# Kernel optimization log

Hardware: AMD Instinct MI355X
Metric: run time of the kernel (lower is better)

Reference implementation:

```python
import jax, jax.numpy as jnp
import numpy as np
from jax import lax

PIXEL_MAX = 255.0  # PSNR reference intensity, matches I=255 in the torch source


def setup_inputs() -> dict:
    key = jax.random.key(0)
    k1, k2 = jax.random.split(key)
    # RGBA image and RGBA kernel, 0..255 pixel range (PSNR uses I=255)
    x = jax.random.uniform(k1, (1, 4, 2048, 2048), dtype=jnp.float32) * PIXEL_MAX
    kernel = jax.random.uniform(k2, (1, 4, 16, 16), dtype=jnp.float32) * PIXEL_MAX
    return {"x": x, "kernel": kernel}


def reference(x, kernel):
    """Fused equivalent of: unfold every (Hk,Wk) window, alpha-blend it with the
    kernel using the kernel's alpha channel, then per-window PSNR vs the kernel.

    alpha_blend(x_win, k, a) = (1-a)*x_win + a*k  with a = k_alpha/255, so
    blended - k = (1-a)*(x_win - k), hence per-window per-channel MSE is a
    weighted sliding-window sum: mean_ij w_ij*(x-k)^2 with w = (1-a)^2.
    Expanding (x-k)^2 lets us use three depthwise VALID correlations instead of
    materializing the [L,C,Hk,Wk] unfold+repeat tensor.
    """
    C, Hk, Wk = kernel.shape[1], kernel.shape[2], kernel.shape[3]
    k = kernel[0]                       # (C, Hk, Wk)
    alpha = k[3] / PIXEL_MAX            # (Hk, Wk), alpha plane (channel 3)
    w = (1.0 - alpha) ** 2              # per-tap weight, shared across channels

    dn = ("NCHW", "OIHW", "NCHW")
    w_dw = jnp.broadcast_to(w, (C, 1, Hk, Wk))   # depthwise weights
    kw_dw = (k * w)[:, None]                      # (C, 1, Hk, Wk)

    def corr(inp, wt):
        return lax.conv_general_dilated(
            inp, wt, window_strides=(1, 1), padding="VALID",
            dimension_numbers=dn, feature_group_count=C)

    Sxx = corr(x * x, w_dw)                        # (1, C, H', W') sum w*x^2
    Sxk = corr(x, kw_dw)                           # (1, C, H', W') sum w*x*k
    Skk = jnp.sum(k * k * w, axis=(-2, -1))[None, :, None, None]  # sum w*k^2

    mse = (Sxx - 2.0 * Sxk + Skk) / (Hk * Wk)      # (1, C, H', W')
    psnr = jnp.mean(20.0 * jnp.log10(PIXEL_MAX / jnp.sqrt(mse)), axis=1)  # mean over C
    return psnr[0]                                  # (H-Hk+1, W-Wk+1)
```

## Files before the change

kernel.cpp:

```cpp
#include <hip/hip_runtime.h>
#include <hip/hip_bf16.h>
#include <math.h>

#define XDIM 2048
#define OW   2033
#define TR   32
#define TC   256
#define NIP  47
#define XW   272

typedef __bf16 bf16x8 __attribute__((ext_vector_type(8)));
typedef float  f32x16 __attribute__((ext_vector_type(16)));

union U128 { uint4 u; bf16x8 v; };

__device__ __forceinline__ unsigned short bfbits(float f) {
    return __builtin_bit_cast(unsigned short, __float2bfloat16(f));
}
__device__ __forceinline__ unsigned int packx(float f) {
    return ((unsigned int)bfbits(f) << 16) | (unsigned int)bfbits(f * f);
}

__global__ __launch_bounds__(256) void psnr_mfma_kernel(
    const float* __restrict__ x,
    const float* __restrict__ kern,
    float* __restrict__ out)
{
    __shared__ __align__(16) unsigned int xt[NIP * XW];
    __shared__ __align__(16) unsigned int wt[4][17][20];
    __shared__ float skkArr[4];

    const int tid  = threadIdx.x;
    const int lane = tid & 63;
    const int wv   = tid >> 6;
    const int nn   = lane & 31;
    const int hf   = lane >> 5;

    {
        float k0 = kern[tid], k1 = kern[256 + tid], k2 = kern[512 + tid], k3 = kern[768 + tid];
        float a  = k3 * (1.0f / 255.0f);
        float om = 1.0f - a;
        float w  = om * om;
        int i = tid >> 4, j = tid & 15;
        unsigned int wlo = (unsigned int)bfbits(w);
        wt[0][i][j] = ((unsigned int)bfbits(-2.0f * w * k0) << 16) | wlo;
        wt[1][i][j] = ((unsigned int)bfbits(-2.0f * w * k1) << 16) | wlo;
        wt[2][i][j] = ((unsigned int)bfbits(-2.0f * w * k2) << 16) | wlo;
        wt[3][i][j] = ((unsigned int)bfbits(-2.0f * w * k3) << 16) | wlo;
        if (tid < 80) {
            int c = tid / 20, wd = tid % 20;
            wt[c][16][wd] = 0u;
        }
        float4* red = reinterpret_cast<float4*>(xt);
        red[tid] = make_float4(w*k0*k0, w*k1*k1, w*k2*k2, w*k3*k3);
        __syncthreads();
        #pragma unroll
        for (int s = 128; s > 0; s >>= 1) {
            if (tid < s) {
                float4 o = red[tid + s], m = red[tid];
                m.x += o.x; m.y += o.y; m.z += o.z; m.w += o.w;
                red[tid] = m;
            }
            __syncthreads();
        }
        if (tid == 0) {
            float4 r0v = red[0];
            skkArr[0] = r0v.x; skkArr[1] = r0v.y; skkArr[2] = r0v.z; skkArr[3] = r0v.w;
        }
    }

    const int r0 = blockIdx.y * TR;
    const int c0 = blockIdx.x * TC;

    f32x16 psum0 = {0.f}, psum1 = {0.f};
    #pragma unroll
    for (int q = 0; q < 16; ++q) { psum0[q] = 0.0f; psum1[q] = 0.0f; }

    for (int ch = 0; ch < 4; ++ch) {
        __syncthreads();
        const float* __restrict__ xc = x + (size_t)ch * XDIM * XDIM;
        for (int idx = tid; idx < NIP * 68; idx += 256) {
            int row = idx / 68;
            int q4  = (idx - row * 68) * 4;
            int gr  = r0 + row; if (gr > XDIM - 1) gr = XDIM - 1;
            int gc  = c0 + q4;
            const float* rp = xc + (size_t)gr * XDIM;
            float4 v;
            if (gc + 3 <= XDIM - 1) {
                v = *reinterpret_cast<const float4*>(rp + gc);
            } else {
                int e0 = gc     < XDIM ? gc     : XDIM - 1;
                int e1 = gc + 1 < XDIM ? gc + 1 : XDIM - 1;
                int e2 = gc + 2 < XDIM ? gc + 2 : XDIM - 1;
                int e3 = gc + 3 < XDIM ? gc + 3 : XDIM - 1;
                v = make_float4(rp[e0], rp[e1], rp[e2], rp[e3]);
            }
            uint4 pr;
            pr.x = packx(v.x); pr.y = packx(v.y); pr.z = packx(v.z); pr.w = packx(v.w);
            *reinterpret_cast<uint4*>(&xt[row * XW + q4]) = pr;
        }
        __syncthreads();

        f32x16 acc0 = {0.f}, acc1 = {0.f};
        #pragma unroll
        for (int q = 0; q < 16; ++q) { acc0[q] = 0.0f; acc1[q] = 0.0f; }

        for (int ip = 0; ip < NIP; ++ip) {
            unsigned int d = (unsigned int)(ip - nn);
            unsigned int wrow = (d > 15u) ? 16u : d;
            U128 alo, ahi;
            alo.u = *reinterpret_cast<const uint4*>(&wt[ch][wrow][hf * 4]);
            ahi.u = *reinterpret_cast<const uint4*>(&wt[ch][wrow][8 + hf * 4]);

            int xb = ip * XW + nn + hf * 4 + (wv << 6);
            U128 blo0, bhi0, blo1, bhi1;
            blo0.u = make_uint4(xt[xb],      xt[xb + 1],  xt[xb + 2],  xt[xb + 3]);
            bhi0.u = make_uint4(xt[xb + 8],  xt[xb + 9],  xt[xb + 10], xt[xb + 11]);
            blo1.u = make_uint4(xt[xb + 32], xt[xb + 33], xt[xb + 34], xt[xb + 35]);
            bhi1.u = make_uint4(xt[xb + 40], xt[xb + 41], xt[xb + 42], xt[xb + 43]);

            acc0 = __builtin_amdgcn_mfma_f32_32x32x16_bf16(alo.v, blo0.v, acc0, 0, 0, 0);
            acc0 = __builtin_amdgcn_mfma_f32_32x32x16_bf16(ahi.v, bhi0.v, acc0, 0, 0, 0);
            acc1 = __builtin_amdgcn_mfma_f32_32x32x16_bf16(alo.v, blo1.v, acc1, 0, 0, 0);
            acc1 = __builtin_amdgcn_mfma_f32_32x32x16_bf16(ahi.v, bhi1.v, acc1, 0, 0, 0);
        }

        float sk = skkArr[ch];
        #pragma unroll
        for (int q = 0; q < 16; ++q) {
            float m0 = (acc0[q] + sk) * (1.0f / 256.0f);
            float m1 = (acc1[q] + sk) * (1.0f / 256.0f);
            psum0[q] += log10f(m0);
            psum1[q] += log10f(m1);
        }
    }

    const float BASE = 48.130803608679344f;
    const int col0 = c0 + (wv << 6) + nn;
    const int col1 = col0 + 32;
    #pragma unroll
    for (int q = 0; q < 16; ++q) {
        int row = r0 + (q & 3) + ((q >> 2) << 3) + (hf << 2);
        if (row < OW) {
            float* orow = out + (size_t)row * OW;
            if (col0 < OW) orow[col0] = BASE - 2.5f * psum0[q];
            if (col1 < OW) orow[col1] = BASE - 2.5f * psum1[q];
        }
    }
}

extern "C" void kernel_launch(void* const* d_in, const int* in_sizes, int n_in,
                              void* d_out, int out_size, void* d_ws, size_t ws_size,
                              hipStream_t stream) {
    (void)in_sizes; (void)n_in; (void)d_ws; (void)ws_size; (void)out_size;
    const float* x    = (const float*)d_in[0];
    const float* kern = (const float*)d_in[1];
    float* out        = (float*)d_out;

    dim3 grid(XDIM / TC, (OW + TR - 1) / TR);
    psnr_mfma_kernel<<<grid, 256, 0, stream>>>(x, kern, out);
}
```

Measured before the change: 70.61 us.

## Pipeline input staging through triple-buffered row chunks with register prefetch

Replaces the per-channel load-everything-then-compute scheme with 8-row chunks staged through a triple-buffered LDS ring. Global loads for chunk g+3 are issued into registers while chunk g+2 is packed into LDS and chunk g runs MFMA, so memory latency overlaps compute. The LDS layout also changes to pre-duplicated uint2 pairs, so each B operand is built from two 64-bit reads instead of four scalar reads. In exchange it adds a barrier per chunk, more register pressure from the prefetch buffers, and somewhat more LDS write traffic because values are duplicated.

```diff
diff --git a/kernel.cpp b/kernel.cpp
--- a/kernel.cpp
+++ b/kernel.cpp
@@ -6,8 +6,10 @@
 #define OW   2033
 #define TR   32
 #define TC   256
-#define NIP  47
 #define XW   272
+#define CH   8
+#define NCHUNK 6
+#define NG   24
 
 typedef __bf16 bf16x8 __attribute__((ext_vector_type(8)));
 typedef float  f32x16 __attribute__((ext_vector_type(16)));
@@ -26,7 +28,7 @@
     const float* __restrict__ kern,
     float* __restrict__ out)
 {
-    __shared__ __align__(16) unsigned int xt[NIP * XW];
+    __shared__ __align__(16) uint2 bufT[3][CH][XW];
     __shared__ __align__(16) unsigned int wt[4][17][20];
     __shared__ float skkArr[4];
 
@@ -51,7 +53,7 @@
             int c = tid / 20, wd = tid % 20;
             wt[c][16][wd] = 0u;
         }
-        float4* red = reinterpret_cast<float4*>(xt);
+        float4* red = reinterpret_cast<float4*>(&bufT[0][0][0]);
         red[tid] = make_float4(w*k0*k0, w*k1*k1, w*k2*k2, w*k3*k3);
         __syncthreads();
         #pragma unroll
@@ -67,72 +69,127 @@
             float4 r0v = red[0];
             skkArr[0] = r0v.x; skkArr[1] = r0v.y; skkArr[2] = r0v.z; skkArr[3] = r0v.w;
         }
+        __syncthreads();
     }
 
     const int r0 = blockIdx.y * TR;
     const int c0 = blockIdx.x * TC;
 
-    f32x16 psum0 = {0.f}, psum1 = {0.f};
+    float4 sv4[2][3];
+    float  sv1[2][3];
+
+    auto stage_issue = [&](int g, int rs) {
+        int c  = g % NCHUNK;
+        int ch = g / NCHUNK;
+        const float* __restrict__ xc = x + (size_t)ch * XDIM * XDIM;
+        #pragma unroll
+        for (int t = 0; t < 3; ++t) {
+            int idx = tid + 256 * t;
+            if (idx < CH * 68) {
+                int lr = idx / 68;
+                int q4 = (idx - lr * 68) * 4;
+                int gr = r0 + c * CH + lr; if (gr > XDIM - 1) gr = XDIM - 1;
+                int gc = c0 + q4;
+                const float* rp = xc + (size_t)gr * XDIM;
+                float4 v;
+                if (gc + 3 <= XDIM - 1) {
+                    v = *reinterpret_cast<const float4*>(rp + gc);
+                } else {
+                    int e0 = gc     < XDIM ? gc     : XDIM - 1;
+                    int e1 = gc + 1 < XDIM ? gc + 1 : XDIM - 1;
+                    int e2 = gc + 2 < XDIM ? gc + 2 : XDIM - 1;
+                    int e3 = gc + 3 < XDIM ? gc + 3 : XDIM - 1;
+                    v = make_float4(rp[e0], rp[e1], rp[e2], rp[e3]);
+                }
+                int g4 = gc + 4 < XDIM ? gc + 4 : XDIM - 1;
+                sv4[rs][t] = v;
+                sv1[rs][t] = rp[g4];
+            }
+        }
+    };
+
+    auto stage_write = [&](int g, int rs) {
+        int b = g % 3;
+        #pragma unroll
+        for (int t = 0; t < 3; ++t) {
+            int idx = tid + 256 * t;
+            if (idx < CH * 68) {
+                int lr = idx / 68;
+                int q4 = (idx - lr * 68) * 4;
+                float4 v = sv4[rs][t];
+                unsigned int P0 = packx(v.x), P1 = packx(v.y), P2 = packx(v.z),
+                             P3 = packx(v.w), P4 = packx(sv1[rs][t]);
+                uint4* dst = reinterpret_cast<uint4*>(&bufT[b][lr][q4]);
+                dst[0] = make_uint4(P0, P1, P1, P2);
+                dst[1] = make_uint4(P2, P3, P3, P4);
+            }
+        }
+    };
+
+    stage_issue(0, 0);
+    stage_issue(1, 1);
+    stage_write(0, 0);
+    stage_issue(2, 0);
+    stage_write(1, 1);
+    __syncthreads();
+
+    f32x16 acc0, acc1, psum0, psum1;
     #pragma unroll
     for (int q = 0; q < 16; ++q) { psum0[q] = 0.0f; psum1[q] = 0.0f; }
 
-    for (int ch = 0; ch < 4; ++ch) {
+    const int xbase = nn + 4 * hf + (wv << 6);
+
+    for (int g = 0; g < NG; ++g) {
+        const int c  = g % NCHUNK;
+        const int ch = g / NCHUNK;
+
+        if (g + 2 < NG) stage_write(g + 2, g & 1);
+        if (g + 3 < NG) stage_issue(g + 3, (g + 1) & 1);
+
+        if (c == 0) {
+            #pragma unroll
+            for (int q = 0; q < 16; ++q) { acc0[q] = 0.0f; acc1[q] = 0.0f; }
+        }
+
+        const uint2* __restrict__ bp = &bufT[g % 3][0][0];
+        const unsigned int* __restrict__ wch = &wt[ch][0][0];
+
+        #pragma unroll
+        for (int lr = 0; lr < CH; ++lr) {
+            int ip = c * CH + lr;
+            if (ip < 47) {
+                unsigned int d = (unsigned int)(ip - nn);
+                unsigned int wrow = (d > 15u) ? 16u : d;
+                U128 alo, ahi;
+                alo.u = *reinterpret_cast<const uint4*>(wch + wrow * 20 + hf * 4);
+                ahi.u = *reinterpret_cast<const uint4*>(wch + wrow * 20 + 8 + hf * 4);
+
+                int xb = lr * XW + xbase;
+                U128 blo0, bhi0, blo1, bhi1;
+                { uint2 a0 = bp[xb],      a1 = bp[xb + 2];  blo0.u = make_uint4(a0.x, a0.y, a1.x, a1.y); }
+                { uint2 a0 = bp[xb + 8],  a1 = bp[xb + 10]; bhi0.u = make_uint4(a0.x, a0.y, a1.x, a1.y); }
+                { uint2 a0 = bp[xb + 32], a1 = bp[xb + 34]; blo1.u = make_uint4(a0.x, a0.y, a1.x, a1.y); }
+                { uint2 a0 = bp[xb + 40], a1 = bp[xb + 42]; bhi1.u = make_uint4(a0.x, a0.y, a1.x, a1.y); }
+
+                acc0 = __builtin_amdgcn_mfma_f32_32x32x16_bf16(alo.v, blo0.v, acc0, 0, 0, 0);
+                acc0 = __builtin_amdgcn_mfma_f32_32x32x16_bf16(ahi.v, bhi0.v, acc0, 0, 0, 0);
+                acc1 = __builtin_amdgcn_mfma_f32_32x32x16_bf16(alo.v, blo1.v, acc1, 0, 0, 0);
+                acc1 = __builtin_amdgcn_mfma_f32_32x32x16_bf16(ahi.v, bhi1.v, acc1, 0, 0, 0);
+            }
+        }
+
+        if (c == NCHUNK - 1) {
+            float sk = skkArr[ch];
+            #pragma unroll
+            for (int q = 0; q < 16; ++q) {
+                float m0 = (acc0[q] + sk) * (1.0f / 256.0f);
+                float m1 = (acc1[q] + sk) * (1.0f / 256.0f);
+                psum0[q] += log10f(m0);
+                psum1[q] += log10f(m1);
+            }
+        }
+
         __syncthreads();
-        const float* __restrict__ xc = x + (size_t)ch * XDIM * XDIM;
-        for (int idx = tid; idx < NIP * 68; idx += 256) {
-            int row = idx / 68;
-            int q4  = (idx - row * 68) * 4;
-            int gr  = r0 + row; if (gr > XDIM - 1) gr = XDIM - 1;
-            int gc  = c0 + q4;
-            const float* rp = xc + (size_t)gr * XDIM;
-            float4 v;
-            if (gc + 3 <= XDIM - 1) {
-                v = *reinterpret_cast<const float4*>(rp + gc);
-            } else {
-                int e0 = gc     < XDIM ? gc     : XDIM - 1;
-                int e1 = gc + 1 < XDIM ? gc + 1 : XDIM - 1;
-                int e2 = gc + 2 < XDIM ? gc + 2 : XDIM - 1;
-                int e3 = gc + 3 < XDIM ? gc + 3 : XDIM - 1;
-                v = make_float4(rp[e0], rp[e1], rp[e2], rp[e3]);
-            }
-            uint4 pr;
-            pr.x = packx(v.x); pr.y = packx(v.y); pr.z = packx(v.z); pr.w = packx(v.w);
-            *reinterpret_cast<uint4*>(&xt[row * XW + q4]) = pr;
-        }
-        __syncthreads();
-
-        f32x16 acc0 = {0.f}, acc1 = {0.f};
-        #pragma unroll
-        for (int q = 0; q < 16; ++q) { acc0[q] = 0.0f; acc1[q] = 0.0f; }
-
-        for (int ip = 0; ip < NIP; ++ip) {
-            unsigned int d = (unsigned int)(ip - nn);
-            unsigned int wrow = (d > 15u) ? 16u : d;
-            U128 alo, ahi;
-            alo.u = *reinterpret_cast<const uint4*>(&wt[ch][wrow][hf * 4]);
-            ahi.u = *reinterpret_cast<const uint4*>(&wt[ch][wrow][8 + hf * 4]);
-
-            int xb = ip * XW + nn + hf * 4 + (wv << 6);
-            U128 blo0, bhi0, blo1, bhi1;
-            blo0.u = make_uint4(xt[xb],      xt[xb + 1],  xt[xb + 2],  xt[xb + 3]);
-            bhi0.u = make_uint4(xt[xb + 8],  xt[xb + 9],  xt[xb + 10], xt[xb + 11]);
-            blo1.u = make_uint4(xt[xb + 32], xt[xb + 33], xt[xb + 34], xt[xb + 35]);
-            bhi1.u = make_uint4(xt[xb + 40], xt[xb + 41], xt[xb + 42], xt[xb + 43]);
-
-            acc0 = __builtin_amdgcn_mfma_f32_32x32x16_bf16(alo.v, blo0.v, acc0, 0, 0, 0);
-            acc0 = __builtin_amdgcn_mfma_f32_32x32x16_bf16(ahi.v, bhi0.v, acc0, 0, 0, 0);
-            acc1 = __builtin_amdgcn_mfma_f32_32x32x16_bf16(alo.v, blo1.v, acc1, 0, 0, 0);
-            acc1 = __builtin_amdgcn_mfma_f32_32x32x16_bf16(ahi.v, bhi1.v, acc1, 0, 0, 0);
-        }
-
-        float sk = skkArr[ch];
-        #pragma unroll
-        for (int q = 0; q < 16; ++q) {
-            float m0 = (acc0[q] + sk) * (1.0f / 256.0f);
-            float m1 = (acc1[q] + sk) * (1.0f / 256.0f);
-            psum0[q] += log10f(m0);
-            psum1[q] += log10f(m1);
-        }
     }
 
     const float BASE = 48.130803608679344f;
```

New measurement: 115.3 us. 63.3% more time.

## Replace block-wide tile staging with per-wave register-prefetched LDS ring pipeline

Applied to the files above, without the earlier changes.

Drops the per-channel block-wide load of the full 47-row tile and its barriers. Each wave now streams its own 80-column slice row by row into a private 8-slot LDS ring, keeping four global loads in flight in registers while the MFMAs run on earlier rows. Channels and rows are flattened into 188 steps, and the LDS layout changes to pre-expanded uint2 pairs. The goal is to overlap global latency with MFMA work and remove block syncs. In exchange, only 20 lanes per wave issue loads and wave-local LDS reuse depends on implicit wave ordering with no explicit barrier.

```diff
diff --git a/kernel.cpp b/kernel.cpp
--- a/kernel.cpp
+++ b/kernel.cpp
@@ -6,8 +6,9 @@
 #define OW   2033
 #define TR   32
 #define TC   256
-#define NIP  47
-#define XW   272
+#define WPC  80
+#define NROW 47
+#define NG   188
 
 typedef __bf16 bf16x8 __attribute__((ext_vector_type(8)));
 typedef float  f32x16 __attribute__((ext_vector_type(16)));
@@ -26,7 +27,7 @@
     const float* __restrict__ kern,
     float* __restrict__ out)
 {
-    __shared__ __align__(16) unsigned int xt[NIP * XW];
+    __shared__ __align__(16) uint2 ring[4][8][WPC];
     __shared__ __align__(16) unsigned int wt[4][17][20];
     __shared__ float skkArr[4];
 
@@ -35,6 +36,49 @@
     const int wv   = tid >> 6;
     const int nn   = lane & 31;
     const int hf   = lane >> 5;
+
+    const int r0  = blockIdx.y * TR;
+    const int c0  = blockIdx.x * TC;
+    const int c0w = c0 + (wv << 6);
+
+    float4 s04, s14, s24, s34;
+    float  s01, s11, s21, s31;
+
+    auto issue = [&](int g, float4& v4, float& v1) {
+        int ch = (g * 1395) >> 16;
+        int ip = g - 47 * ch;
+        if (lane < 20) {
+            int gr = r0 + ip; if (gr > XDIM - 1) gr = XDIM - 1;
+            int gc = c0w + 4 * lane;
+            const float* rp = x + ((size_t)ch << 22) + (size_t)gr * XDIM;
+            if (gc + 3 <= XDIM - 1) {
+                v4 = *reinterpret_cast<const float4*>(rp + gc);
+            } else {
+                int e0 = gc     < XDIM ? gc     : XDIM - 1;
+                int e1 = gc + 1 < XDIM ? gc + 1 : XDIM - 1;
+                int e2 = gc + 2 < XDIM ? gc + 2 : XDIM - 1;
+                int e3 = gc + 3 < XDIM ? gc + 3 : XDIM - 1;
+                v4 = make_float4(rp[e0], rp[e1], rp[e2], rp[e3]);
+            }
+            int e4 = gc + 4 < XDIM ? gc + 4 : XDIM - 1;
+            v1 = rp[e4];
+        }
+    };
+
+    auto wr = [&](int g, const float4& v4, const float& v1) {
+        if (lane < 20) {
+            unsigned int P0 = packx(v4.x), P1 = packx(v4.y), P2 = packx(v4.z),
+                         P3 = packx(v4.w), P4 = packx(v1);
+            uint4* dst = reinterpret_cast<uint4*>(&ring[wv][g & 7][lane * 4]);
+            dst[0] = make_uint4(P0, P1, P1, P2);
+            dst[1] = make_uint4(P2, P3, P3, P4);
+        }
+    };
+
+    issue(0, s04, s01);
+    issue(1, s14, s11);
+    issue(2, s24, s21);
+    issue(3, s34, s31);
 
     {
         float k0 = kern[tid], k1 = kern[256 + tid], k2 = kern[512 + tid], k3 = kern[768 + tid];
@@ -51,7 +95,7 @@
             int c = tid / 20, wd = tid % 20;
             wt[c][16][wd] = 0u;
         }
-        float4* red = reinterpret_cast<float4*>(xt);
+        float4* red = reinterpret_cast<float4*>(&ring[0][0][0]);
         red[tid] = make_float4(w*k0*k0, w*k1*k1, w*k2*k2, w*k3*k3);
         __syncthreads();
         #pragma unroll
@@ -67,76 +111,76 @@
             float4 r0v = red[0];
             skkArr[0] = r0v.x; skkArr[1] = r0v.y; skkArr[2] = r0v.z; skkArr[3] = r0v.w;
         }
+        __syncthreads();
     }
 
-    const int r0 = blockIdx.y * TR;
-    const int c0 = blockIdx.x * TC;
-
-    f32x16 psum0 = {0.f}, psum1 = {0.f};
+    f32x16 acc0, acc1, psum0, psum1;
     #pragma unroll
     for (int q = 0; q < 16; ++q) { psum0[q] = 0.0f; psum1[q] = 0.0f; }
 
-    for (int ch = 0; ch < 4; ++ch) {
-        __syncthreads();
-        const float* __restrict__ xc = x + (size_t)ch * XDIM * XDIM;
-        for (int idx = tid; idx < NIP * 68; idx += 256) {
-            int row = idx / 68;
-            int q4  = (idx - row * 68) * 4;
-            int gr  = r0 + row; if (gr > XDIM - 1) gr = XDIM - 1;
-            int gc  = c0 + q4;
-            const float* rp = xc + (size_t)gr * XDIM;
-            float4 v;
-            if (gc + 3 <= XDIM - 1) {
-                v = *reinterpret_cast<const float4*>(rp + gc);
-            } else {
-                int e0 = gc     < XDIM ? gc     : XDIM - 1;
-                int e1 = gc + 1 < XDIM ? gc + 1 : XDIM - 1;
-                int e2 = gc + 2 < XDIM ? gc + 2 : XDIM - 1;
-                int e3 = gc + 3 < XDIM ? gc + 3 : XDIM - 1;
-                v = make_float4(rp[e0], rp[e1], rp[e2], rp[e3]);
+    const int xb = nn + 4 * hf;
+
+    auto compute = [&](int g) {
+        int ch = (g * 1395) >> 16;
+        int ip = g - 47 * ch;
+        if (ip == 0) {
+            #pragma unroll
+            for (int q = 0; q < 16; ++q) { acc0[q] = 0.0f; acc1[q] = 0.0f; }
+        }
+        const unsigned int* __restrict__ wch = &wt[ch][0][0];
+        unsigned int d = (unsigned int)(ip - nn);
+        unsigned int wrow = (d > 15u) ? 16u : d;
+        U128 alo, ahi;
+        alo.u = *reinterpret_cast<const uint4*>(wch + wrow * 20 + hf * 4);
+        ahi.u = *reinterpret_cast<const uint4*>(wch + wrow * 20 + 8 + hf * 4);
+
+        const uint2* __restrict__ bp = &ring[wv][g & 7][0];
+        U128 blo0, bhi0, blo1, bhi1;
+        { uint2 a0 = bp[xb],      a1 = bp[xb + 2];  blo0.u = make_uint4(a0.x, a0.y, a1.x, a1.y); }
+        { uint2 a0 = bp[xb + 8],  a1 = bp[xb + 10]; bhi0.u = make_uint4(a0.x, a0.y, a1.x, a1.y); }
+        { uint2 a0 = bp[xb + 32], a1 = bp[xb + 34]; blo1.u = make_uint4(a0.x, a0.y, a1.x, a1.y); }
+        { uint2 a0 = bp[xb + 40], a1 = bp[xb + 42]; bhi1.u = make_uint4(a0.x, a0.y, a1.x, a1.y); }
+
+        acc0 = __builtin_amdgcn_mfma_f32_32x32x16_bf16(alo.v, blo0.v, acc0, 0, 0, 0);
+        acc0 = __builtin_amdgcn_mfma_f32_32x32x16_bf16(ahi.v, bhi0.v, acc0, 0, 0, 0);
+        acc1 = __builtin_amdgcn_mfma_f32_32x32x16_bf16(alo.v, blo1.v, acc1, 0, 0, 0);
+        acc1 = __builtin_amdgcn_mfma_f32_32x32x16_bf16(ahi.v, bhi1.v, acc1, 0, 0, 0);
+
+        if (ip == NROW - 1) {
+            float sk = skkArr[ch];
+            #pragma unroll
+            for (int q = 0; q < 16; ++q) {
+                float m0 = (acc0[q] + sk) * (1.0f / 256.0f);
+                float m1 = (acc1[q] + sk) * (1.0f / 256.0f);
+                psum0[q] += log10f(m0);
+                psum1[q] += log10f(m1);
             }
-            uint4 pr;
-            pr.x = packx(v.x); pr.y = packx(v.y); pr.z = packx(v.z); pr.w = packx(v.w);
-            *reinterpret_cast<uint4*>(&xt[row * XW + q4]) = pr;
-        }
-        __syncthreads();
-
-        f32x16 acc0 = {0.f}, acc1 = {0.f};
-        #pragma unroll
-        for (int q = 0; q < 16; ++q) { acc0[q] = 0.0f; acc1[q] = 0.0f; }
-
-        for (int ip = 0; ip < NIP; ++ip) {
-            unsigned int d = (unsigned int)(ip - nn);
-            unsigned int wrow = (d > 15u) ? 16u : d;
-            U128 alo, ahi;
-            alo.u = *reinterpret_cast<const uint4*>(&wt[ch][wrow][hf * 4]);
-            ahi.u = *reinterpret_cast<const uint4*>(&wt[ch][wrow][8 + hf * 4]);
-
-            int xb = ip * XW + nn + hf * 4 + (wv << 6);
-            U128 blo0, bhi0, blo1, bhi1;
-            blo0.u = make_uint4(xt[xb],      xt[xb + 1],  xt[xb + 2],  xt[xb + 3]);
-            bhi0.u = make_uint4(xt[xb + 8],  xt[xb + 9],  xt[xb + 10], xt[xb + 11]);
-            blo1.u = make_uint4(xt[xb + 32], xt[xb + 33], xt[xb + 34], xt[xb + 35]);
-            bhi1.u = make_uint4(xt[xb + 40], xt[xb + 41], xt[xb + 42], xt[xb + 43]);
-
-            acc0 = __builtin_amdgcn_mfma_f32_32x32x16_bf16(alo.v, blo0.v, acc0, 0, 0, 0);
-            acc0 = __builtin_amdgcn_mfma_f32_32x32x16_bf16(ahi.v, bhi0.v, acc0, 0, 0, 0);
-            acc1 = __builtin_amdgcn_mfma_f32_32x32x16_bf16(alo.v, blo1.v, acc1, 0, 0, 0);
-            acc1 = __builtin_amdgcn_mfma_f32_32x32x16_bf16(ahi.v, bhi1.v, acc1, 0, 0, 0);
-        }
-
-        float sk = skkArr[ch];
-        #pragma unroll
-        for (int q = 0; q < 16; ++q) {
-            float m0 = (acc0[q] + sk) * (1.0f / 256.0f);
-            float m1 = (acc1[q] + sk) * (1.0f / 256.0f);
-            psum0[q] += log10f(m0);
-            psum1[q] += log10f(m1);
-        }
+        }
+    };
+
+    wr(0, s04, s01);
+    issue(4, s04, s01);
+
+    for (int g = 0; g < NG; g += 4) {
+        wr(g + 1, s14, s11);
+        if (g + 5 < NG) issue(g + 5, s14, s11);
+        compute(g);
+
+        wr(g + 2, s24, s21);
+        if (g + 6 < NG) issue(g + 6, s24, s21);
+        compute(g + 1);
+
+        wr(g + 3, s34, s31);
+        if (g + 7 < NG) issue(g + 7, s34, s31);
+        compute(g + 2);
+
+        if (g + 4 < NG) { wr(g + 4, s04, s01); }
+        if (g + 8 < NG) issue(g + 8, s04, s01);
+        compute(g + 3);
     }
 
     const float BASE = 48.130803608679344f;
-    const int col0 = c0 + (wv << 6) + nn;
+    const int col0 = c0w + nn;
     const int col1 = col0 + 32;
     #pragma unroll
     for (int q = 0; q < 16; ++q) {
```

After: 159.7 us. +126.2%, slower.

## Prefetch next channel's tile into registers during MFMA, use fast log2

Applied to the files above, without the earlier changes.

Global loads for the next channel's input tile now go into a 13-entry float4 register buffer and are issued before the MFMA loop of the current channel. The bf16 pack and LDS store happen at the top of the next iteration, so global memory latency overlaps with matrix compute. The per-channel log10f calls are replaced by __log2f, with the output scale folded into a constant. The register buffer adds roughly 52 VGPRs, which may lower occupancy, and __log2f is slightly less accurate.

```diff
diff --git a/kernel.cpp b/kernel.cpp
--- a/kernel.cpp
+++ b/kernel.cpp
@@ -6,8 +6,9 @@
 #define OW   2033
 #define TR   32
 #define TC   256
-#define NIP  47
 #define XW   272
+#define NIT  13
+#define NITEMS (47*68)
 
 typedef __bf16 bf16x8 __attribute__((ext_vector_type(8)));
 typedef float  f32x16 __attribute__((ext_vector_type(16)));
@@ -26,7 +27,7 @@
     const float* __restrict__ kern,
     float* __restrict__ out)
 {
-    __shared__ __align__(16) unsigned int xt[NIP * XW];
+    __shared__ __align__(16) unsigned int xt[47 * XW];
     __shared__ __align__(16) unsigned int wt[4][17][20];
     __shared__ float skkArr[4];
 
@@ -35,6 +36,51 @@
     const int wv   = tid >> 6;
     const int nn   = lane & 31;
     const int hf   = lane >> 5;
+
+    const int r0 = blockIdx.y * TR;
+    const int c0 = blockIdx.x * TC;
+
+    float4 pf[NIT];
+
+    auto issue = [&](int ch) {
+        const float* __restrict__ xc = x + ((size_t)ch << 22);
+        #pragma unroll
+        for (int t = 0; t < NIT; ++t) {
+            int idx = tid + 256 * t;
+            if (idx < NITEMS) {
+                int row = idx / 68;
+                int q4  = (idx - row * 68) * 4;
+                int gr  = r0 + row; if (gr > XDIM - 1) gr = XDIM - 1;
+                int gc  = c0 + q4;
+                const float* rp = xc + (size_t)gr * XDIM;
+                if (gc + 3 <= XDIM - 1) {
+                    pf[t] = *reinterpret_cast<const float4*>(rp + gc);
+                } else {
+                    int e0 = gc     < XDIM ? gc     : XDIM - 1;
+                    int e1 = gc + 1 < XDIM ? gc + 1 : XDIM - 1;
+                    int e2 = gc + 2 < XDIM ? gc + 2 : XDIM - 1;
+                    int e3 = gc + 3 < XDIM ? gc + 3 : XDIM - 1;
+                    pf[t] = make_float4(rp[e0], rp[e1], rp[e2], rp[e3]);
+                }
+            }
+        }
+    };
+
+    auto wrt = [&]() {
+        #pragma unroll
+        for (int t = 0; t < NIT; ++t) {
+            int idx = tid + 256 * t;
+            if (idx < NITEMS) {
+                int row = idx / 68;
+                int q4  = (idx - row * 68) * 4;
+                float4 v = pf[t];
+                *reinterpret_cast<uint4*>(&xt[row * XW + q4]) =
+                    make_uint4(packx(v.x), packx(v.y), packx(v.z), packx(v.w));
+            }
+        }
+    };
+
+    issue(0);
 
     {
         float k0 = kern[tid], k1 = kern[256 + tid], k2 = kern[512 + tid], k3 = kern[768 + tid];
@@ -51,7 +97,7 @@
             int c = tid / 20, wd = tid % 20;
             wt[c][16][wd] = 0u;
         }
-        float4* red = reinterpret_cast<float4*>(xt);
+        float4* red = reinterpret_cast<float4*>(&xt[0]);
         red[tid] = make_float4(w*k0*k0, w*k1*k1, w*k2*k2, w*k3*k3);
         __syncthreads();
         #pragma unroll
@@ -67,52 +113,34 @@
             float4 r0v = red[0];
             skkArr[0] = r0v.x; skkArr[1] = r0v.y; skkArr[2] = r0v.z; skkArr[3] = r0v.w;
         }
+        __syncthreads();
     }
 
-    const int r0 = blockIdx.y * TR;
-    const int c0 = blockIdx.x * TC;
-
-    f32x16 psum0 = {0.f}, psum1 = {0.f};
+    f32x16 psum0, psum1;
     #pragma unroll
     for (int q = 0; q < 16; ++q) { psum0[q] = 0.0f; psum1[q] = 0.0f; }
 
+    const int xbase = nn + 4 * hf + (wv << 6);
+
     for (int ch = 0; ch < 4; ++ch) {
+        wrt();
         __syncthreads();
-        const float* __restrict__ xc = x + (size_t)ch * XDIM * XDIM;
-        for (int idx = tid; idx < NIP * 68; idx += 256) {
-            int row = idx / 68;
-            int q4  = (idx - row * 68) * 4;
-            int gr  = r0 + row; if (gr > XDIM - 1) gr = XDIM - 1;
-            int gc  = c0 + q4;
-            const float* rp = xc + (size_t)gr * XDIM;
-            float4 v;
-            if (gc + 3 <= XDIM - 1) {
-                v = *reinterpret_cast<const float4*>(rp + gc);
-            } else {
-                int e0 = gc     < XDIM ? gc     : XDIM - 1;
-                int e1 = gc + 1 < XDIM ? gc + 1 : XDIM - 1;
-                int e2 = gc + 2 < XDIM ? gc + 2 : XDIM - 1;
-                int e3 = gc + 3 < XDIM ? gc + 3 : XDIM - 1;
-                v = make_float4(rp[e0], rp[e1], rp[e2], rp[e3]);
-            }
-            uint4 pr;
-            pr.x = packx(v.x); pr.y = packx(v.y); pr.z = packx(v.z); pr.w = packx(v.w);
-            *reinterpret_cast<uint4*>(&xt[row * XW + q4]) = pr;
-        }
-        __syncthreads();
+        if (ch < 3) issue(ch + 1);
 
-        f32x16 acc0 = {0.f}, acc1 = {0.f};
+        f32x16 acc0, acc1;
         #pragma unroll
         for (int q = 0; q < 16; ++q) { acc0[q] = 0.0f; acc1[q] = 0.0f; }
 
-        for (int ip = 0; ip < NIP; ++ip) {
+        const unsigned int* __restrict__ wch = &wt[ch][0][0];
+
+        for (int ip = 0; ip < 47; ++ip) {
             unsigned int d = (unsigned int)(ip - nn);
             unsigned int wrow = (d > 15u) ? 16u : d;
             U128 alo, ahi;
-            alo.u = *reinterpret_cast<const uint4*>(&wt[ch][wrow][hf * 4]);
-            ahi.u = *reinterpret_cast<const uint4*>(&wt[ch][wrow][8 + hf * 4]);
+            alo.u = *reinterpret_cast<const uint4*>(wch + wrow * 20 + hf * 4);
+            ahi.u = *reinterpret_cast<const uint4*>(wch + wrow * 20 + 8 + hf * 4);
 
-            int xb = ip * XW + nn + hf * 4 + (wv << 6);
+            int xb = ip * XW + xbase;
             U128 blo0, bhi0, blo1, bhi1;
             blo0.u = make_uint4(xt[xb],      xt[xb + 1],  xt[xb + 2],  xt[xb + 3]);
             bhi0.u = make_uint4(xt[xb + 8],  xt[xb + 9],  xt[xb + 10], xt[xb + 11]);
@@ -130,12 +158,15 @@
         for (int q = 0; q < 16; ++q) {
             float m0 = (acc0[q] + sk) * (1.0f / 256.0f);
             float m1 = (acc1[q] + sk) * (1.0f / 256.0f);
-            psum0[q] += log10f(m0);
-            psum1[q] += log10f(m1);
+            psum0[q] += __log2f(m0);
+            psum1[q] += __log2f(m1);
         }
+
+        __syncthreads();
     }
 
     const float BASE = 48.130803608679344f;
+    const float SC   = 2.5f * 0.3010299956639812f;
     const int col0 = c0 + (wv << 6) + nn;
     const int col1 = col0 + 32;
     #pragma unroll
@@ -143,8 +174,8 @@
         int row = r0 + (q & 3) + ((q >> 2) << 3) + (hf << 2);
         if (row < OW) {
             float* orow = out + (size_t)row * OW;
-            if (col0 < OW) orow[col0] = BASE - 2.5f * psum0[q];
-            if (col1 < OW) orow[col1] = BASE - 2.5f * psum1[q];
+            if (col0 < OW) orow[col0] = BASE - SC * psum0[q];
+            if (col1 < OW) orow[col1] = BASE - SC * psum1[q];
         }
     }
 }
```

New measurement: 95.31 us. 1.35x slower.
